# Kernel tuning notes

Measured on AMD Instinct MI355X. Metric: run time of the kernel, lower is better.

Reference implementation:

```python
import jax, jax.numpy as jnp
import numpy as np

B, T, C = 2, 2048, 768
H = 12
D = C // H  # head size = 64
F = 4 * C
EPS = 1e-5


def _layernorm(x, g, b):
    mu = jnp.mean(x, axis=-1, keepdims=True)
    var = jnp.var(x, axis=-1, keepdims=True)
    return (x - mu) * jax.lax.rsqrt(var + EPS) * g + b


def setup_inputs() -> dict:
    key = jax.random.key(0)
    ks = jax.random.split(key, 16)
    s_in = 1.0 / np.sqrt(C)
    s_ff = 1.0 / np.sqrt(F)
    return {
        "x": jax.random.normal(ks[0], (B, T, C), dtype=jnp.float32),
        # per-head projection weights, stacked [H, C, D] (no bias, as in nn.Linear(bias=False))
        "Wq": jax.random.uniform(ks[1], (H, C, D), jnp.float32, -s_in, s_in),
        "Wk": jax.random.uniform(ks[2], (H, C, D), jnp.float32, -s_in, s_in),
        "Wv": jax.random.uniform(ks[3], (H, C, D), jnp.float32, -s_in, s_in),
        "Wp": jax.random.uniform(ks[4], (C, C), jnp.float32, -s_in, s_in),
        "bp": jax.random.uniform(ks[5], (C,), jnp.float32, -s_in, s_in),
        "W1": jax.random.uniform(ks[6], (C, F), jnp.float32, -s_in, s_in),
        "b1": jax.random.uniform(ks[7], (F,), jnp.float32, -s_in, s_in),
        "W2": jax.random.uniform(ks[8], (F, C), jnp.float32, -s_ff, s_ff),
        "b2": jax.random.uniform(ks[9], (C,), jnp.float32, -s_ff, s_ff),
        "ln1_g": jnp.ones((C,), jnp.float32),
        "ln1_b": jnp.zeros((C,), jnp.float32),
        "ln2_g": jnp.ones((C,), jnp.float32),
        "ln2_b": jnp.zeros((C,), jnp.float32),
    }


def reference(x, Wq, Wk, Wv, Wp, bp, W1, b1, W2, b2, ln1_g, ln1_b, ln2_g, ln2_b):
    # --- self-attention sublayer (pre-LN) ---
    h = _layernorm(x, ln1_g, ln1_b)                      # [B,T,C]
    q = jnp.einsum('btc,hcd->bhtd', h, Wq)
    k = jnp.einsum('btc,hcd->bhtd', h, Wk)
    v = jnp.einsum('btc,hcd->bhtd', h, Wv)
    # NOTE: original scales by C**-0.5 where C = n_embd (full width), not head size
    scale = C ** (-0.5)
    wei = jnp.einsum('bhtd,bhsd->bhts', q, k) * scale    # [B,H,T,T]
    causal = jnp.tril(jnp.ones((T, T), dtype=bool))
    wei = jnp.where(causal, wei, -jnp.inf)
    wei = jax.nn.softmax(wei, axis=-1)
    out = jnp.einsum('bhts,bhsd->bhtd', wei, v)          # [B,H,T,D]
    out = out.transpose(0, 2, 1, 3).reshape(B, T, C)     # concat heads
    sa = out @ Wp + bp
    x = x + sa
    # --- feed-forward sublayer (pre-LN); ReLU after BOTH linears, as in source ---
    h2 = _layernorm(x, ln2_g, ln2_b)
    ff = jax.nn.relu(jax.nn.relu(h2 @ W1 + b1) @ W2 + b2)
    return x + ff
```

## Files before the change

kernel.cpp:

```cpp
#include <hip/hip_runtime.h>
#include <hip/hip_bf16.h>

#define TSEQ 2048
#define CDIM 768
#define NHEAD 12
#define DHEAD 64
#define FDIM 3072
#define MROWS 4096
#define BH 24

typedef __attribute__((ext_vector_type(8))) short short8;
typedef __attribute__((ext_vector_type(4))) float f32x4;

__device__ inline unsigned short f2bf(float f) {
  __hip_bfloat16 h = __float2bfloat16(f);
  return __builtin_bit_cast(unsigned short, h);
}
__device__ inline float bf2f(unsigned short u) {
  unsigned int v = ((unsigned int)u) << 16;
  return __builtin_bit_cast(float, v);
}

__device__ inline void gload16(const unsigned short* g, unsigned short* l) {
  __builtin_amdgcn_global_load_lds(
      (const __attribute__((address_space(1))) unsigned int*)g,
      (__attribute__((address_space(3))) unsigned int*)l, 16, 0, 0);
}

__global__ __launch_bounds__(256) void prep_all(
    const float* __restrict__ Wq, const float* __restrict__ Wk,
    const float* __restrict__ Wv, const float* __restrict__ Wp,
    const float* __restrict__ W1, const float* __restrict__ W2,
    unsigned short* __restrict__ WqkvT, unsigned short* __restrict__ WpT,
    unsigned short* __restrict__ W1T, unsigned short* __restrict__ W2T,
    const float* __restrict__ x, const float* __restrict__ ln1g,
    const float* __restrict__ ln1b, unsigned short* __restrict__ h1) {
  __shared__ float tile[32][33];
  __shared__ float red[8];
  int b = blockIdx.x;
  if (b >= 6912) {
    int row = b - 6912;
    int tid = threadIdx.x;
    const float* xr = x + (size_t)row * CDIM;
    float v[3];
    float s = 0.f;
#pragma unroll
    for (int i = 0; i < 3; ++i) { v[i] = xr[tid + i * 256]; s += v[i]; }
#pragma unroll
    for (int m = 1; m < 64; m <<= 1) s += __shfl_xor(s, m);
    int w = tid >> 6;
    if ((tid & 63) == 0) red[w] = s;
    __syncthreads();
    float mean = (red[0] + red[1] + red[2] + red[3]) * (1.f / CDIM);
    float vs = 0.f;
#pragma unroll
    for (int i = 0; i < 3; ++i) { float d = v[i] - mean; vs += d * d; }
#pragma unroll
    for (int m = 1; m < 64; m <<= 1) vs += __shfl_xor(vs, m);
    if ((tid & 63) == 0) red[4 + w] = vs;
    __syncthreads();
    float var = (red[4] + red[5] + red[6] + red[7]) * (1.f / CDIM);
    float rstd = rsqrtf(var + 1e-5f);
    unsigned short* orow = h1 + (size_t)row * CDIM;
#pragma unroll
    for (int i = 0; i < 3; ++i) {
      int c = tid + i * 256;
      orow[c] = f2bf((v[i] - mean) * rstd * ln1g[c] + ln1b[c]);
    }
    return;
  }
  int xx = threadIdx.x & 31, y = threadIdx.x >> 5;
  if (b < 1728) {
    int cx = b % 24, dy = (b / 24) % 2, ph = b / 48;
    int proj = ph / NHEAD, h = ph % NHEAD;
    const float* in = (proj == 0 ? Wq : (proj == 1 ? Wk : Wv)) + (size_t)h * CDIM * DHEAD;
    int c0 = cx * 32, d0 = dy * 32;
#pragma unroll
    for (int i = 0; i < 4; ++i)
      tile[y + i * 8][xx] = in[(size_t)(c0 + y + i * 8) * DHEAD + d0 + xx];
    __syncthreads();
#pragma unroll
    for (int i = 0; i < 4; ++i)
      WqkvT[(size_t)(proj * CDIM + h * DHEAD + d0 + y + i * 8) * CDIM + c0 + xx] =
          f2bf(tile[xx][y + i * 8]);
  } else {
    const float* in;
    unsigned short* out;
    int R, C, bx, by;
    if (b < 2304) {
      int b2 = b - 1728;
      in = Wp; out = WpT; R = CDIM; C = CDIM; bx = b2 % 24; by = b2 / 24;
    } else if (b < 4608) {
      int b2 = b - 2304;
      in = W1; out = W1T; R = CDIM; C = FDIM; bx = b2 % 96; by = b2 / 96;
    } else {
      int b2 = b - 4608;
      in = W2; out = W2T; R = FDIM; C = CDIM; bx = b2 % 24; by = b2 / 24;
    }
    int c0 = bx * 32, r0 = by * 32;
#pragma unroll
    for (int i = 0; i < 4; ++i)
      tile[y + i * 8][xx] = in[(size_t)(r0 + y + i * 8) * C + c0 + xx];
    __syncthreads();
#pragma unroll
    for (int i = 0; i < 4; ++i)
      out[(size_t)(c0 + y + i * 8) * R + r0 + xx] = f2bf(tile[xx][y + i * 8]);
  }
}

__global__ __launch_bounds__(256) void ln_kernel(
    const float* __restrict__ x, const float* __restrict__ g,
    const float* __restrict__ b, unsigned short* __restrict__ out) {
  int row = blockIdx.x;
  int tid = threadIdx.x;
  const float* xr = x + (size_t)row * CDIM;
  float v[3];
  float s = 0.f;
#pragma unroll
  for (int i = 0; i < 3; ++i) { v[i] = xr[tid + i * 256]; s += v[i]; }
#pragma unroll
  for (int m = 1; m < 64; m <<= 1) s += __shfl_xor(s, m);
  __shared__ float red[8];
  int w = tid >> 6;
  if ((tid & 63) == 0) red[w] = s;
  __syncthreads();
  float mean = (red[0] + red[1] + red[2] + red[3]) * (1.f / CDIM);
  float vs = 0.f;
#pragma unroll
  for (int i = 0; i < 3; ++i) { float d = v[i] - mean; vs += d * d; }
#pragma unroll
  for (int m = 1; m < 64; m <<= 1) vs += __shfl_xor(vs, m);
  if ((tid & 63) == 0) red[4 + w] = vs;
  __syncthreads();
  float var = (red[4] + red[5] + red[6] + red[7]) * (1.f / CDIM);
  float rstd = rsqrtf(var + 1e-5f);
  unsigned short* orow = out + (size_t)row * CDIM;
#pragma unroll
  for (int i = 0; i < 3; ++i) {
    int c = tid + i * 256;
    orow[c] = f2bf((v[i] - mean) * rstd * g[c] + b[c]);
  }
}

template <int EPI, int SPLITK = 1>
__global__ __launch_bounds__(256) void gemm_bt(
    const unsigned short* __restrict__ A, const unsigned short* __restrict__ BT,
    int M, int N, int K,
    const float* __restrict__ bias, const float* __restrict__ aux,
    float* __restrict__ outf, unsigned short* __restrict__ outb,
    unsigned short* __restrict__ qo, unsigned short* __restrict__ ko,
    unsigned short* __restrict__ vo) {
  constexpr int SH_CNT = (EPI == 0) ? 128 * 136 : 2 * 128 * 64;
  __shared__ unsigned short sh[SH_CNT];
  unsigned short* As = sh;
  unsigned short* Bs = sh + 128 * 64;
  int tid = threadIdx.x;
  int lane = tid & 63, wave = tid >> 6;
  int wr = wave >> 1, wc = wave & 1;
  int l15 = lane & 15, lg = lane >> 4;
  int lr = lane >> 3, lc = lane & 7;
  int chunk = gridDim.x >> 3;
  int logical = (blockIdx.x & 7) * chunk + (blockIdx.x >> 3);
  int mt = M >> 7;
  int tiles = mt * (N >> 7);
  int split = logical / tiles;
  int tl = logical % tiles;
  size_t bm = (size_t)(tl % mt) * 128, bn = (size_t)(tl / mt) * 128;
  int Ks = K / SPLITK;
  int kbeg = split * Ks, kend = kbeg + Ks;
  f32x4 acc[4][4] = {};

  for (int kt = kbeg; kt < kend; kt += 64) {
#pragma unroll
    for (int i = 0; i < 4; ++i) {
      int r0 = (wave * 4 + i) * 8;
      gload16(A + (bm + r0 + lr) * K + kt + (lc ^ lr) * 8, &As[r0 * 64]);
      gload16(BT + (bn + r0 + lr) * K + kt + (lc ^ lr) * 8, &Bs[r0 * 64]);
    }
    __syncthreads();
    __builtin_amdgcn_s_setprio(1);
#pragma unroll
    for (int kk = 0; kk < 64; kk += 32) {
      int kb = kk + lg * 8;
      short8 af[4], bfr[4];
#pragma unroll
      for (int m = 0; m < 4; ++m) {
        int row = wr * 64 + m * 16 + l15;
        af[m] = *reinterpret_cast<const short8*>(&As[row * 64 + (kb ^ ((row & 7) << 3))]);
      }
#pragma unroll
      for (int n = 0; n < 4; ++n) {
        int row = wc * 64 + n * 16 + l15;
        bfr[n] = *reinterpret_cast<const short8*>(&Bs[row * 64 + (kb ^ ((row & 7) << 3))]);
      }
#pragma unroll
      for (int m = 0; m < 4; ++m)
#pragma unroll
        for (int n = 0; n < 4; ++n)
          acc[m][n] = __builtin_amdgcn_mfma_f32_16x16x32_bf16(af[m], bfr[n], acc[m][n], 0, 0, 0);
    }
    __builtin_amdgcn_s_setprio(0);
    __syncthreads();
  }

  if constexpr (EPI == 0) {
    if (bn >= 1536) {
#pragma unroll
      for (int m = 0; m < 4; ++m)
#pragma unroll
        for (int n = 0; n < 4; ++n)
#pragma unroll
          for (int r = 0; r < 4; ++r) {
            int rowL = wr * 64 + m * 16 + lg * 4 + r;
            int c = wc * 64 + n * 16 + l15;
            sh[c * 136 + rowL] = f2bf(acc[m][n][r]);
          }
      __syncthreads();
      int bb = (int)(bm >> 11);
      int t0g = (int)(bm & 2047);
      int vbase = (int)bn - 1536;
#pragma unroll
      for (int it = 0; it < 8; ++it) {
        int ch = it * 256 + tid;
        int c = ch >> 4, tlc = (ch & 15) * 8;
        int vcol = vbase + c;
        int hh = vcol >> 6, dd = vcol & 63;
        *reinterpret_cast<int4*>(
            vo + (((size_t)(bb * NHEAD + hh)) * DHEAD + dd) * TSEQ + t0g + tlc) =
            *reinterpret_cast<const int4*>(&sh[c * 136 + tlc]);
      }
    } else {
#pragma unroll
      for (int m = 0; m < 4; ++m)
#pragma unroll
        for (int n = 0; n < 4; ++n)
#pragma unroll
          for (int r = 0; r < 4; ++r) {
            int row = (int)bm + wr * 64 + m * 16 + lg * 4 + r;
            int col = (int)bn + wc * 64 + n * 16 + l15;
            float val = acc[m][n][r];
            int proj = col / CDIM, rem = col % CDIM;
            int h = rem >> 6, d = rem & 63;
            int b = row >> 11, t = row & (TSEQ - 1);
            if (proj == 0) {
              qo[(((size_t)(b * NHEAD + h)) * TSEQ + t) * DHEAD + d] =
                  f2bf(val * 0.05205877247186126f);
            } else {
              ko[(((size_t)(b * NHEAD + h)) * TSEQ + t) * DHEAD + d] = f2bf(val);
            }
          }
    }
  } else {
#pragma unroll
    for (int m = 0; m < 4; ++m) {
#pragma unroll
      for (int n = 0; n < 4; ++n) {
#pragma unroll
        for (int r = 0; r < 4; ++r) {
          int row = (int)bm + wr * 64 + m * 16 + lg * 4 + r;
          int col = (int)bn + wc * 64 + n * 16 + l15;
          float val = acc[m][n][r];
          if constexpr (EPI == 1) {
            size_t idx = (size_t)row * CDIM + col;
            outf[idx] = val + bias[col] + aux[idx];
          } else if constexpr (EPI == 2) {
            size_t idx = (size_t)row * FDIM + col;
            outb[idx] = f2bf(fmaxf(val + bias[col], 0.f));
          } else if constexpr (EPI == 3) {
            size_t idx = (size_t)row * CDIM + col;
            outf[idx] = aux[idx] + fmaxf(val + bias[col], 0.f);
          } else {
            outb[(size_t)split * M * N + (size_t)row * N + col] = f2bf(val);
          }
        }
      }
    }
  }
}

template <int NPART, bool RELU>
__global__ __launch_bounds__(256) void reduce_k(
    const unsigned short* __restrict__ part,
    const float* __restrict__ bias, const float* __restrict__ aux,
    float* __restrict__ out) {
  int e = (blockIdx.x * 256 + threadIdx.x) * 4;
  int col = e % CDIM;
  float4 xv = *reinterpret_cast<const float4*>(aux + e);
  float4 bv = *reinterpret_cast<const float4*>(bias + col);
  float s0 = 0.f, s1 = 0.f, s2 = 0.f, s3 = 0.f;
#pragma unroll
  for (int p = 0; p < NPART; ++p) {
    short4 pv = *reinterpret_cast<const short4*>(part + (size_t)p * MROWS * CDIM + e);
    s0 += bf2f((unsigned short)pv.x);
    s1 += bf2f((unsigned short)pv.y);
    s2 += bf2f((unsigned short)pv.z);
    s3 += bf2f((unsigned short)pv.w);
  }
  float4 ov;
  if constexpr (RELU) {
    ov.x = xv.x + fmaxf(s0 + bv.x, 0.f);
    ov.y = xv.y + fmaxf(s1 + bv.y, 0.f);
    ov.z = xv.z + fmaxf(s2 + bv.z, 0.f);
    ov.w = xv.w + fmaxf(s3 + bv.w, 0.f);
  } else {
    ov.x = xv.x + s0 + bv.x;
    ov.y = xv.y + s1 + bv.y;
    ov.z = xv.z + s2 + bv.z;
    ov.w = xv.w + s3 + bv.w;
  }
  *reinterpret_cast<float4*>(out + e) = ov;
}

__global__ __launch_bounds__(256) void attn_kernel(
    const unsigned short* __restrict__ Q, const unsigned short* __restrict__ Kd,
    const unsigned short* __restrict__ VT, unsigned short* __restrict__ O) {
  __shared__ unsigned short Kl[3][64 * 64];
  __shared__ unsigned short Vl[3][64 * 64];
  __shared__ unsigned short plds[4][16 * 64];
  int tid = threadIdx.x;
  int wave = tid >> 6, lane = tid & 63;
  int l15 = lane & 15, lg = lane >> 4;
  int bid = blockIdx.x;
  int xcd = bid & 7, idx = bid >> 3;
  int bh = xcd * 3 + idx / 16;
  int p = idx & 15;
  const unsigned short* qp = Q + (size_t)bh * TSEQ * DHEAD;
  const unsigned short* kp = Kd + (size_t)bh * TSEQ * DHEAD;
  const unsigned short* vp = VT + (size_t)bh * DHEAD * TSEQ;
  unsigned short* pw = plds[wave];
  int b = bh / NHEAD, h = bh % NHEAD;

  short8 ones;
  {
    unsigned short ov = (l15 == 0) ? (unsigned short)0x3F80 : (unsigned short)0;
#pragma unroll
    for (int j = 0; j < 8; ++j) ones[j] = (short)ov;
  }

  int lr = lane >> 3, lc = lane & 7;
  int jsw = lc ^ lr;

  auto stage = [&](int t, int buf) {
    int s0 = t * 64;
#pragma unroll
    for (int i = 0; i < 2; ++i) {
      int r0 = (wave * 2 + i) * 8;
      gload16(kp + (size_t)(s0 + r0 + lr) * DHEAD + jsw * 8, &Kl[buf][r0 * 64]);
      gload16(vp + (size_t)(r0 + lr) * TSEQ + s0 + jsw * 8, &Vl[buf][r0 * 64]);
    }
  };

  auto run_stripe = [&](int stripe) {
    int qbase = stripe * 64 + wave * 16;
    int nt = stripe + 1;
    short8 qf[2];
#pragma unroll
    for (int kk = 0; kk < 2; ++kk)
      qf[kk] = *reinterpret_cast<const short8*>(
          qp + (size_t)(qbase + l15) * DHEAD + kk * 32 + lg * 8);
    f32x4 oacc[5] = {};

    stage(0, 0);
    if (nt > 1) {
      stage(1, 1);
      asm volatile("s_waitcnt vmcnt(4)" ::: "memory");
    } else {
      asm volatile("s_waitcnt vmcnt(0)" ::: "memory");
    }
    __builtin_amdgcn_s_barrier();

    for (int t = 0; t < nt; ++t) {
      int cur = t % 3;
      bool pre2 = (t + 2 < nt);
      if (pre2) stage(t + 2, (t + 2) % 3);
      int s0 = t * 64;
      f32x4 sacc[4] = {};
      __builtin_amdgcn_s_setprio(1);
#pragma unroll
      for (int st = 0; st < 4; ++st) {
        int row = st * 16 + l15;
        int sw = row & 7;
#pragma unroll
        for (int kk = 0; kk < 2; ++kk) {
          short8 kf = *reinterpret_cast<const short8*>(
              &Kl[cur][row * 64 + (((kk * 4 + lg) ^ sw) * 8)]);
          sacc[st] = __builtin_amdgcn_mfma_f32_16x16x32_bf16(qf[kk], kf, sacc[st], 0, 0, 0);
        }
      }
      __builtin_amdgcn_s_setprio(0);
      bool last = (t == nt - 1);
#pragma unroll
      for (int r = 0; r < 4; ++r) {
        int qrow = qbase + lg * 4 + r;
        int prow = lg * 4 + r;
        int psw = (prow & 7) << 3;
        if (last) {
#pragma unroll
          for (int st = 0; st < 4; ++st) {
            float pv = exp2f(sacc[st][r]);
            if (s0 + st * 16 + l15 > qrow) pv = 0.f;
            pw[prow * 64 + ((st * 16 + l15) ^ psw)] = f2bf(pv);
          }
        } else {
#pragma unroll
          for (int st = 0; st < 4; ++st)
            pw[prow * 64 + ((st * 16 + l15) ^ psw)] = f2bf(exp2f(sacc[st][r]));
        }
      }
      int prsw = (l15 & 7) << 3;
      short8 pa0 = *reinterpret_cast<const short8*>(&pw[l15 * 64 + ((lg * 8) ^ prsw)]);
      short8 pa1 = *reinterpret_cast<const short8*>(&pw[l15 * 64 + ((32 + lg * 8) ^ prsw)]);
      __builtin_amdgcn_s_setprio(1);
#pragma unroll
      for (int n = 0; n < 4; ++n) {
        int row = n * 16 + l15;
        int sw = row & 7;
        short8 vf0 = *reinterpret_cast<const short8*>(&Vl[cur][row * 64 + ((lg ^ sw) * 8)]);
        oacc[n] = __builtin_amdgcn_mfma_f32_16x16x32_bf16(pa0, vf0, oacc[n], 0, 0, 0);
        short8 vf1 = *reinterpret_cast<const short8*>(&Vl[cur][row * 64 + (((4 + lg) ^ sw) * 8)]);
        oacc[n] = __builtin_amdgcn_mfma_f32_16x16x32_bf16(pa1, vf1, oacc[n], 0, 0, 0);
      }
      oacc[4] = __builtin_amdgcn_mfma_f32_16x16x32_bf16(pa0, ones, oacc[4], 0, 0, 0);
      oacc[4] = __builtin_amdgcn_mfma_f32_16x16x32_bf16(pa1, ones, oacc[4], 0, 0, 0);
      __builtin_amdgcn_s_setprio(0);
      if (pre2) asm volatile("s_waitcnt vmcnt(4)" ::: "memory");
      else      asm volatile("s_waitcnt vmcnt(0)" ::: "memory");
      __builtin_amdgcn_s_barrier();
    }

#pragma unroll
    for (int r = 0; r < 4; ++r) {
      float lsum = __shfl(oacc[4][r], lane & 48);
      float inv = 1.f / lsum;
      int row = qbase + lg * 4 + r;
#pragma unroll
      for (int n = 0; n < 4; ++n)
        O[(size_t)(b * TSEQ + row) * CDIM + h * DHEAD + n * 16 + l15] =
            f2bf(oacc[n][r] * inv);
    }
  };

  run_stripe(31 - p);
  run_stripe(p);
}

extern "C" void kernel_launch(void* const* d_in, const int* in_sizes, int n_in,
                              void* d_out, int out_size, void* d_ws, size_t ws_size,
                              hipStream_t stream) {
  const float* x    = (const float*)d_in[0];
  const float* Wq   = (const float*)d_in[1];
  const float* Wk   = (const float*)d_in[2];
  const float* Wv   = (const float*)d_in[3];
  const float* Wp   = (const float*)d_in[4];
  const float* bp   = (const float*)d_in[5];
  const float* W1   = (const float*)d_in[6];
  const float* b1   = (const float*)d_in[7];
  const float* W2   = (const float*)d_in[8];
  const float* b2   = (const float*)d_in[9];
  const float* ln1g = (const float*)d_in[10];
  const float* ln1b = (const float*)d_in[11];
  const float* ln2g = (const float*)d_in[12];
  const float* ln2b = (const float*)d_in[13];
  float* out = (float*)d_out;

  char* ws = (char*)d_ws;
  auto alloc = [&](size_t bytes) {
    char* p = ws;
    ws += (bytes + 255) & ~(size_t)255;
    return p;
  };
  unsigned short* h1    = (unsigned short*)alloc((size_t)MROWS * CDIM * 2);
  unsigned short* WqkvT = (unsigned short*)alloc((size_t)3 * CDIM * CDIM * 2);
  unsigned short* WpT   = (unsigned short*)alloc((size_t)CDIM * CDIM * 2);
  unsigned short* W1T   = (unsigned short*)alloc((size_t)FDIM * CDIM * 2);
  unsigned short* W2T   = (unsigned short*)alloc((size_t)CDIM * FDIM * 2);
  unsigned short* Qb    = (unsigned short*)alloc((size_t)BH * TSEQ * DHEAD * 2);
  unsigned short* Kb    = (unsigned short*)alloc((size_t)BH * TSEQ * DHEAD * 2);
  unsigned short* VTb   = (unsigned short*)alloc((size_t)BH * TSEQ * DHEAD * 2);
  unsigned short* AO    = (unsigned short*)alloc((size_t)MROWS * CDIM * 2);
  float*          x1    = (float*)alloc((size_t)MROWS * CDIM * 4);
  unsigned short* h2    = (unsigned short*)alloc((size_t)MROWS * CDIM * 2);
  unsigned short* a1    = (unsigned short*)alloc((size_t)MROWS * FDIM * 2);
  unsigned short* partP = Qb;

  prep_all<<<11008, 256, 0, stream>>>(Wq, Wk, Wv, Wp, W1, W2,
                                      WqkvT, WpT, W1T, W2T, x, ln1g, ln1b, h1);
  gemm_bt<0><<<576, 256, 0, stream>>>(h1, WqkvT, MROWS, 3 * CDIM, CDIM,
                                      nullptr, nullptr, nullptr, nullptr, Qb, Kb, VTb);
  attn_kernel<<<384, 256, 0, stream>>>(Qb, Kb, VTb, AO);
  gemm_bt<4, 2><<<384, 256, 0, stream>>>(AO, WpT, MROWS, CDIM, CDIM,
                                         nullptr, nullptr, nullptr, partP,
                                         nullptr, nullptr, nullptr);
  reduce_k<2, false><<<3072, 256, 0, stream>>>(partP, bp, x, x1);
  ln_kernel<<<4096, 256, 0, stream>>>(x1, ln2g, ln2b, h2);
  gemm_bt<2><<<768, 256, 0, stream>>>(h2, W1T, MROWS, FDIM, CDIM,
                                      b1, nullptr, nullptr, a1, nullptr, nullptr, nullptr);
  gemm_bt<4, 4><<<768, 256, 0, stream>>>(a1, W2T, MROWS, CDIM, FDIM,
                                         nullptr, nullptr, nullptr, partP,
                                         nullptr, nullptr, nullptr);
  reduce_k<4, true><<<3072, 256, 0, stream>>>(partP, b2, x1, out);
}
```

Measured before the change: 164.2 us.

## Software-pipeline attention PV behind next QK and fuse split-K reduce with LayerNorm

In the attention kernel, P·V for tile t-1 now runs after the QK^T for tile t is issued. P is double-buffered per wave and K is double-buffered, while V stays triple-buffered, so the softmax exp of one tile can overlap the MFMA work of the neighbouring one. Prefetch depth drops from two tiles ahead to one, with a full vmcnt(0) wait each iteration. Separately, the split-K reduction of the projection output, the bias and the residual add are fused into the LN2 kernel. This removes one launch and one round trip of x1 through memory, but the wait may expose more load latency.

```diff
diff --git a/kernel.cpp b/kernel.cpp
--- a/kernel.cpp
+++ b/kernel.cpp
@@ -108,16 +108,24 @@
   }
 }
 
-__global__ __launch_bounds__(256) void ln_kernel(
-    const float* __restrict__ x, const float* __restrict__ g,
-    const float* __restrict__ b, unsigned short* __restrict__ out) {
+__global__ __launch_bounds__(256) void redln(
+    const unsigned short* __restrict__ part,
+    const float* __restrict__ bias, const float* __restrict__ x,
+    float* __restrict__ x1, const float* __restrict__ g,
+    const float* __restrict__ bb, unsigned short* __restrict__ h2) {
   int row = blockIdx.x;
   int tid = threadIdx.x;
-  const float* xr = x + (size_t)row * CDIM;
   float v[3];
   float s = 0.f;
 #pragma unroll
-  for (int i = 0; i < 3; ++i) { v[i] = xr[tid + i * 256]; s += v[i]; }
+  for (int i = 0; i < 3; ++i) {
+    int c = tid + i * 256;
+    size_t idx = (size_t)row * CDIM + c;
+    float t = bf2f(part[idx]) + bf2f(part[(size_t)MROWS * CDIM + idx]) + bias[c] + x[idx];
+    v[i] = t;
+    x1[idx] = t;
+    s += t;
+  }
 #pragma unroll
   for (int m = 1; m < 64; m <<= 1) s += __shfl_xor(s, m);
   __shared__ float red[8];
@@ -134,11 +142,11 @@
   __syncthreads();
   float var = (red[4] + red[5] + red[6] + red[7]) * (1.f / CDIM);
   float rstd = rsqrtf(var + 1e-5f);
-  unsigned short* orow = out + (size_t)row * CDIM;
+  unsigned short* orow = h2 + (size_t)row * CDIM;
 #pragma unroll
   for (int i = 0; i < 3; ++i) {
     int c = tid + i * 256;
-    orow[c] = f2bf((v[i] - mean) * rstd * g[c] + b[c]);
+    orow[c] = f2bf((v[i] - mean) * rstd * g[c] + bb[c]);
   }
 }
 
@@ -314,9 +322,9 @@
 __global__ __launch_bounds__(256) void attn_kernel(
     const unsigned short* __restrict__ Q, const unsigned short* __restrict__ Kd,
     const unsigned short* __restrict__ VT, unsigned short* __restrict__ O) {
-  __shared__ unsigned short Kl[3][64 * 64];
+  __shared__ unsigned short Kl[2][64 * 64];
   __shared__ unsigned short Vl[3][64 * 64];
-  __shared__ unsigned short plds[4][16 * 64];
+  __shared__ unsigned short plds[4][2][16 * 64];
   int tid = threadIdx.x;
   int wave = tid >> 6, lane = tid & 63;
   int l15 = lane & 15, lg = lane >> 4;
@@ -327,7 +335,6 @@
   const unsigned short* qp = Q + (size_t)bh * TSEQ * DHEAD;
   const unsigned short* kp = Kd + (size_t)bh * TSEQ * DHEAD;
   const unsigned short* vp = VT + (size_t)bh * DHEAD * TSEQ;
-  unsigned short* pw = plds[wave];
   int b = bh / NHEAD, h = bh % NHEAD;
 
   short8 ones;
@@ -340,12 +347,19 @@
   int lr = lane >> 3, lc = lane & 7;
   int jsw = lc ^ lr;
 
-  auto stage = [&](int t, int buf) {
+  auto stageK = [&](int t, int buf) {
     int s0 = t * 64;
 #pragma unroll
     for (int i = 0; i < 2; ++i) {
       int r0 = (wave * 2 + i) * 8;
       gload16(kp + (size_t)(s0 + r0 + lr) * DHEAD + jsw * 8, &Kl[buf][r0 * 64]);
+    }
+  };
+  auto stageV = [&](int t, int buf) {
+    int s0 = t * 64;
+#pragma unroll
+    for (int i = 0; i < 2; ++i) {
+      int r0 = (wave * 2 + i) * 8;
       gload16(vp + (size_t)(r0 + lr) * TSEQ + s0 + jsw * 8, &Vl[buf][r0 * 64]);
     }
   };
@@ -360,21 +374,40 @@
           qp + (size_t)(qbase + l15) * DHEAD + kk * 32 + lg * 8);
     f32x4 oacc[5] = {};
 
-    stage(0, 0);
-    if (nt > 1) {
-      stage(1, 1);
-      asm volatile("s_waitcnt vmcnt(4)" ::: "memory");
-    } else {
-      asm volatile("s_waitcnt vmcnt(0)" ::: "memory");
-    }
+    auto pv = [&](int tpv) {
+      const unsigned short* pb = plds[wave][tpv & 1];
+      int vb = tpv % 3;
+      int prsw = (l15 & 7) << 3;
+      short8 pa0 = *reinterpret_cast<const short8*>(&pb[l15 * 64 + ((lg * 8) ^ prsw)]);
+      short8 pa1 = *reinterpret_cast<const short8*>(&pb[l15 * 64 + ((32 + lg * 8) ^ prsw)]);
+      __builtin_amdgcn_s_setprio(1);
+#pragma unroll
+      for (int n = 0; n < 4; ++n) {
+        int row = n * 16 + l15;
+        int sw = row & 7;
+        short8 vf0 = *reinterpret_cast<const short8*>(&Vl[vb][row * 64 + ((lg ^ sw) * 8)]);
+        oacc[n] = __builtin_amdgcn_mfma_f32_16x16x32_bf16(pa0, vf0, oacc[n], 0, 0, 0);
+        short8 vf1 = *reinterpret_cast<const short8*>(&Vl[vb][row * 64 + (((4 + lg) ^ sw) * 8)]);
+        oacc[n] = __builtin_amdgcn_mfma_f32_16x16x32_bf16(pa1, vf1, oacc[n], 0, 0, 0);
+      }
+      oacc[4] = __builtin_amdgcn_mfma_f32_16x16x32_bf16(pa0, ones, oacc[4], 0, 0, 0);
+      oacc[4] = __builtin_amdgcn_mfma_f32_16x16x32_bf16(pa1, ones, oacc[4], 0, 0, 0);
+      __builtin_amdgcn_s_setprio(0);
+    };
+
+    stageK(0, 0);
+    stageV(0, 0);
+    asm volatile("s_waitcnt vmcnt(0)" ::: "memory");
     __builtin_amdgcn_s_barrier();
 
     for (int t = 0; t < nt; ++t) {
-      int cur = t % 3;
-      bool pre2 = (t + 2 < nt);
-      if (pre2) stage(t + 2, (t + 2) % 3);
-      int s0 = t * 64;
+      if (t + 1 < nt) {
+        stageV(t + 1, (t + 1) % 3);
+        stageK(t + 1, (t + 1) & 1);
+      }
+      if (t > 0) pv(t - 1);
       f32x4 sacc[4] = {};
+      int kb = t & 1;
       __builtin_amdgcn_s_setprio(1);
 #pragma unroll
       for (int st = 0; st < 4; ++st) {
@@ -383,12 +416,14 @@
 #pragma unroll
         for (int kk = 0; kk < 2; ++kk) {
           short8 kf = *reinterpret_cast<const short8*>(
-              &Kl[cur][row * 64 + (((kk * 4 + lg) ^ sw) * 8)]);
+              &Kl[kb][row * 64 + (((kk * 4 + lg) ^ sw) * 8)]);
           sacc[st] = __builtin_amdgcn_mfma_f32_16x16x32_bf16(qf[kk], kf, sacc[st], 0, 0, 0);
         }
       }
       __builtin_amdgcn_s_setprio(0);
+      unsigned short* pw = plds[wave][t & 1];
       bool last = (t == nt - 1);
+      int s0 = t * 64;
 #pragma unroll
       for (int r = 0; r < 4; ++r) {
         int qrow = qbase + lg * 4 + r;
@@ -397,9 +432,9 @@
         if (last) {
 #pragma unroll
           for (int st = 0; st < 4; ++st) {
-            float pv = exp2f(sacc[st][r]);
-            if (s0 + st * 16 + l15 > qrow) pv = 0.f;
-            pw[prow * 64 + ((st * 16 + l15) ^ psw)] = f2bf(pv);
+            float pvx = exp2f(sacc[st][r]);
+            if (s0 + st * 16 + l15 > qrow) pvx = 0.f;
+            pw[prow * 64 + ((st * 16 + l15) ^ psw)] = f2bf(pvx);
           }
         } else {
 #pragma unroll
@@ -407,26 +442,10 @@
             pw[prow * 64 + ((st * 16 + l15) ^ psw)] = f2bf(exp2f(sacc[st][r]));
         }
       }
-      int prsw = (l15 & 7) << 3;
-      short8 pa0 = *reinterpret_cast<const short8*>(&pw[l15 * 64 + ((lg * 8) ^ prsw)]);
-      short8 pa1 = *reinterpret_cast<const short8*>(&pw[l15 * 64 + ((32 + lg * 8) ^ prsw)]);
-      __builtin_amdgcn_s_setprio(1);
-#pragma unroll
-      for (int n = 0; n < 4; ++n) {
-        int row = n * 16 + l15;
-        int sw = row & 7;
-        short8 vf0 = *reinterpret_cast<const short8*>(&Vl[cur][row * 64 + ((lg ^ sw) * 8)]);
-        oacc[n] = __builtin_amdgcn_mfma_f32_16x16x32_bf16(pa0, vf0, oacc[n], 0, 0, 0);
-        short8 vf1 = *reinterpret_cast<const short8*>(&Vl[cur][row * 64 + (((4 + lg) ^ sw) * 8)]);
-        oacc[n] = __builtin_amdgcn_mfma_f32_16x16x32_bf16(pa1, vf1, oacc[n], 0, 0, 0);
-      }
-      oacc[4] = __builtin_amdgcn_mfma_f32_16x16x32_bf16(pa0, ones, oacc[4], 0, 0, 0);
-      oacc[4] = __builtin_amdgcn_mfma_f32_16x16x32_bf16(pa1, ones, oacc[4], 0, 0, 0);
-      __builtin_amdgcn_s_setprio(0);
-      if (pre2) asm volatile("s_waitcnt vmcnt(4)" ::: "memory");
-      else      asm volatile("s_waitcnt vmcnt(0)" ::: "memory");
+      asm volatile("s_waitcnt vmcnt(0)" ::: "memory");
       __builtin_amdgcn_s_barrier();
     }
+    pv(nt - 1);
 
 #pragma unroll
     for (int r = 0; r < 4; ++r) {
@@ -491,8 +510,7 @@
   gemm_bt<4, 2><<<384, 256, 0, stream>>>(AO, WpT, MROWS, CDIM, CDIM,
                                          nullptr, nullptr, nullptr, partP,
                                          nullptr, nullptr, nullptr);
-  reduce_k<2, false><<<3072, 256, 0, stream>>>(partP, bp, x, x1);
-  ln_kernel<<<4096, 256, 0, stream>>>(x1, ln2g, ln2b, h2);
+  redln<<<4096, 256, 0, stream>>>(partP, bp, x, x1, ln2g, ln2b, h2);
   gemm_bt<2><<<768, 256, 0, stream>>>(h2, W1T, MROWS, FDIM, CDIM,
                                       b1, nullptr, nullptr, a1, nullptr, nullptr, nullptr);
   gemm_bt<4, 4><<<768, 256, 0, stream>>>(a1, W2T, MROWS, CDIM, FDIM,
```

After: 165.5 us. Within noise of the previous version (+0.8%).

## Split attention into 32-row query stripes with 2-wave blocks; fuse split-K reduce with LayerNorm

Applied to the files above, without the earlier changes.

The attention kernel now runs 768 blocks of 128 threads, each handling two 32-row query stripes (paired long/short for causal balance) instead of two 64-row stripes per 4-wave block. This gives finer-grained parallelism and better load balance across CUs. Each wave now stages twice as many K/V rows, and the vmcnt waits are adjusted to match. Separately, the split-K partial reduction, bias add and residual add are fused into the second LayerNorm kernel, which removes one launch and one round trip of x1 through memory.

```diff
diff --git a/kernel.cpp b/kernel.cpp
--- a/kernel.cpp
+++ b/kernel.cpp
@@ -108,16 +108,24 @@
   }
 }
 
-__global__ __launch_bounds__(256) void ln_kernel(
-    const float* __restrict__ x, const float* __restrict__ g,
-    const float* __restrict__ b, unsigned short* __restrict__ out) {
+__global__ __launch_bounds__(256) void redln(
+    const unsigned short* __restrict__ part,
+    const float* __restrict__ bias, const float* __restrict__ x,
+    float* __restrict__ x1, const float* __restrict__ g,
+    const float* __restrict__ bb, unsigned short* __restrict__ h2) {
   int row = blockIdx.x;
   int tid = threadIdx.x;
-  const float* xr = x + (size_t)row * CDIM;
   float v[3];
   float s = 0.f;
 #pragma unroll
-  for (int i = 0; i < 3; ++i) { v[i] = xr[tid + i * 256]; s += v[i]; }
+  for (int i = 0; i < 3; ++i) {
+    int c = tid + i * 256;
+    size_t idx = (size_t)row * CDIM + c;
+    float t = bf2f(part[idx]) + bf2f(part[(size_t)MROWS * CDIM + idx]) + bias[c] + x[idx];
+    v[i] = t;
+    x1[idx] = t;
+    s += t;
+  }
 #pragma unroll
   for (int m = 1; m < 64; m <<= 1) s += __shfl_xor(s, m);
   __shared__ float red[8];
@@ -134,11 +142,11 @@
   __syncthreads();
   float var = (red[4] + red[5] + red[6] + red[7]) * (1.f / CDIM);
   float rstd = rsqrtf(var + 1e-5f);
-  unsigned short* orow = out + (size_t)row * CDIM;
+  unsigned short* orow = h2 + (size_t)row * CDIM;
 #pragma unroll
   for (int i = 0; i < 3; ++i) {
     int c = tid + i * 256;
-    orow[c] = f2bf((v[i] - mean) * rstd * g[c] + b[c]);
+    orow[c] = f2bf((v[i] - mean) * rstd * g[c] + bb[c]);
   }
 }
 
@@ -311,19 +319,19 @@
   *reinterpret_cast<float4*>(out + e) = ov;
 }
 
-__global__ __launch_bounds__(256) void attn_kernel(
+__global__ __launch_bounds__(128) void attn_kernel(
     const unsigned short* __restrict__ Q, const unsigned short* __restrict__ Kd,
     const unsigned short* __restrict__ VT, unsigned short* __restrict__ O) {
   __shared__ unsigned short Kl[3][64 * 64];
   __shared__ unsigned short Vl[3][64 * 64];
-  __shared__ unsigned short plds[4][16 * 64];
+  __shared__ unsigned short plds[2][16 * 64];
   int tid = threadIdx.x;
   int wave = tid >> 6, lane = tid & 63;
   int l15 = lane & 15, lg = lane >> 4;
   int bid = blockIdx.x;
   int xcd = bid & 7, idx = bid >> 3;
-  int bh = xcd * 3 + idx / 16;
-  int p = idx & 15;
+  int bh = xcd * 3 + idx / 32;
+  int s = idx & 31;
   const unsigned short* qp = Q + (size_t)bh * TSEQ * DHEAD;
   const unsigned short* kp = Kd + (size_t)bh * TSEQ * DHEAD;
   const unsigned short* vp = VT + (size_t)bh * DHEAD * TSEQ;
@@ -343,16 +351,16 @@
   auto stage = [&](int t, int buf) {
     int s0 = t * 64;
 #pragma unroll
-    for (int i = 0; i < 2; ++i) {
-      int r0 = (wave * 2 + i) * 8;
+    for (int i = 0; i < 4; ++i) {
+      int r0 = (wave * 4 + i) * 8;
       gload16(kp + (size_t)(s0 + r0 + lr) * DHEAD + jsw * 8, &Kl[buf][r0 * 64]);
       gload16(vp + (size_t)(r0 + lr) * TSEQ + s0 + jsw * 8, &Vl[buf][r0 * 64]);
     }
   };
 
   auto run_stripe = [&](int stripe) {
-    int qbase = stripe * 64 + wave * 16;
-    int nt = stripe + 1;
+    int qbase = stripe * 32 + wave * 16;
+    int nt = (stripe + 2) >> 1;
     short8 qf[2];
 #pragma unroll
     for (int kk = 0; kk < 2; ++kk)
@@ -363,7 +371,7 @@
     stage(0, 0);
     if (nt > 1) {
       stage(1, 1);
-      asm volatile("s_waitcnt vmcnt(4)" ::: "memory");
+      asm volatile("s_waitcnt vmcnt(8)" ::: "memory");
     } else {
       asm volatile("s_waitcnt vmcnt(0)" ::: "memory");
     }
@@ -423,7 +431,7 @@
       oacc[4] = __builtin_amdgcn_mfma_f32_16x16x32_bf16(pa0, ones, oacc[4], 0, 0, 0);
       oacc[4] = __builtin_amdgcn_mfma_f32_16x16x32_bf16(pa1, ones, oacc[4], 0, 0, 0);
       __builtin_amdgcn_s_setprio(0);
-      if (pre2) asm volatile("s_waitcnt vmcnt(4)" ::: "memory");
+      if (pre2) asm volatile("s_waitcnt vmcnt(8)" ::: "memory");
       else      asm volatile("s_waitcnt vmcnt(0)" ::: "memory");
       __builtin_amdgcn_s_barrier();
     }
@@ -440,8 +448,8 @@
     }
   };
 
-  run_stripe(31 - p);
-  run_stripe(p);
+  run_stripe(63 - s);
+  run_stripe(s);
 }
 
 extern "C" void kernel_launch(void* const* d_in, const int* in_sizes, int n_in,
@@ -487,12 +495,11 @@
                                       WqkvT, WpT, W1T, W2T, x, ln1g, ln1b, h1);
   gemm_bt<0><<<576, 256, 0, stream>>>(h1, WqkvT, MROWS, 3 * CDIM, CDIM,
                                       nullptr, nullptr, nullptr, nullptr, Qb, Kb, VTb);
-  attn_kernel<<<384, 256, 0, stream>>>(Qb, Kb, VTb, AO);
+  attn_kernel<<<768, 128, 0, stream>>>(Qb, Kb, VTb, AO);
   gemm_bt<4, 2><<<384, 256, 0, stream>>>(AO, WpT, MROWS, CDIM, CDIM,
                                          nullptr, nullptr, nullptr, partP,
                                          nullptr, nullptr, nullptr);
-  reduce_k<2, false><<<3072, 256, 0, stream>>>(partP, bp, x, x1);
-  ln_kernel<<<4096, 256, 0, stream>>>(x1, ln2g, ln2b, h2);
+  redln<<<4096, 256, 0, stream>>>(partP, bp, x, x1, ln2g, ln2b, h2);
   gemm_bt<2><<<768, 256, 0, stream>>>(h2, W1T, MROWS, FDIM, CDIM,
                                       b1, nullptr, nullptr, a1, nullptr, nullptr, nullptr);
   gemm_bt<4, 4><<<768, 256, 0, stream>>>(a1, W2T, MROWS, CDIM, FDIM,
```

Measured after the change: 163.7 us. No clear change (-0.3%).
